# Optimization experiments

Hardware: AMD Instinct MI355X
Metric: run time of the kernel (lower is better)

Reference implementation:

```python
import jax, jax.numpy as jnp
import numpy as np

N_NODES = 50000
N_EDGES = 400000
D = 512
LN_EPS = 1e-5


def setup_inputs() -> dict:
    key = jax.random.key(0)
    k0, k1, k2, k3 = jax.random.split(key, 4)
    x = jax.random.normal(k0, (N_NODES, D), dtype=jnp.float32)
    src = jax.random.randint(k1, (N_EDGES,), 0, N_NODES, dtype=jnp.int64)
    dst = jax.random.randint(k2, (N_EDGES,), 0, N_NODES, dtype=jnp.int64)
    W = jax.random.normal(k3, (D, D), dtype=jnp.float32) * 0.05
    b = jnp.zeros((D,), dtype=jnp.float32)
    gamma = jnp.ones((D,), dtype=jnp.float32)
    beta = jnp.zeros((D,), dtype=jnp.float32)
    return {"x": x, "W": W, "b": b, "gamma": gamma, "beta": beta, "src": src, "dst": dst}


def reference(x, W, b, gamma, beta, src, dst):
    n = x.shape[0]
    ones = jnp.ones(src.shape, dtype=x.dtype)
    # DGL GraphConv norm='both': clamp degrees to >= 1
    deg_out = jnp.clip(jax.ops.segment_sum(ones, src, num_segments=n), 1.0)  # [N]
    deg_in = jnp.clip(jax.ops.segment_sum(ones, dst, num_segments=n), 1.0)   # [N]
    h = x * jax.lax.rsqrt(deg_out)[:, None]                 # [N, D] src normalization
    agg = jax.ops.segment_sum(h[src], dst, num_segments=n)  # gather->scatter-add SpMM
    h = agg * jax.lax.rsqrt(deg_in)[:, None]                # dst normalization
    h = h @ W + b                                           # dense linear
    # LayerNorm over last dim
    mu = jnp.mean(h, axis=-1, keepdims=True)
    var = jnp.mean(jnp.square(h - mu), axis=-1, keepdims=True)
    h = (h - mu) * jax.lax.rsqrt(var + LN_EPS) * gamma + beta
    # torch nn.GELU default = exact erf GELU
    return jax.nn.gelu(h, approximate=False)
```

## Files before the change

kernel.cpp:

```cpp
#include <hip/hip_runtime.h>
#include <hip/hip_bf16.h>

#define D 512

typedef __attribute__((ext_vector_type(8))) short bf16x8;
typedef __attribute__((ext_vector_type(4))) float f32x4;

__device__ inline float b2f(short h) {
    union { unsigned u; float f; } c;
    c.u = ((unsigned)(unsigned short)h) << 16;
    return c.f;
}

__device__ __forceinline__ void stage16(const void* g, void* l) {
    __builtin_amdgcn_global_load_lds((const __attribute__((address_space(1))) void*)g,
                                     (__attribute__((address_space(3))) void*)l, 16, 0, 0);
}

__global__ void k_hist(const int* __restrict__ src, const int* __restrict__ dst,
                       int* __restrict__ deg_out, int* __restrict__ deg_in, int E) {
    int e = blockIdx.x * 256 + threadIdx.x;
    if (e < E) {
        atomicAdd(&deg_out[src[e]], 1);
        atomicAdd(&deg_in[dst[e]], 1);
    }
}

__global__ __launch_bounds__(256)
void k_scale(const float* __restrict__ x, const int* __restrict__ deg_out,
             __hip_bfloat16* __restrict__ xs, int total16) {
    int i = blockIdx.x * 256 + threadIdx.x;
    if (i >= total16) return;
    int node = i >> 6;
    float w = rsqrtf((float)max(deg_out[node], 1));
    const float4* p = (const float4*)(x + (size_t)i * 8);
    float4 a = p[0], b = p[1];
    union { float4 f4; __hip_bfloat16 h[8]; } o;
    o.h[0] = __float2bfloat16(a.x * w);
    o.h[1] = __float2bfloat16(a.y * w);
    o.h[2] = __float2bfloat16(a.z * w);
    o.h[3] = __float2bfloat16(a.w * w);
    o.h[4] = __float2bfloat16(b.x * w);
    o.h[5] = __float2bfloat16(b.y * w);
    o.h[6] = __float2bfloat16(b.z * w);
    o.h[7] = __float2bfloat16(b.w * w);
    *(float4*)(xs + (size_t)i * 8) = o.f4;
}

__global__ void k_scan1(const int* __restrict__ deg_in, int* __restrict__ row_start,
                        int* __restrict__ partials, int N) {
    __shared__ int sm[1024];
    int tid = threadIdx.x;
    int i = blockIdx.x * 1024 + tid;
    int v = (i < N) ? deg_in[i] : 0;
    sm[tid] = v;
    __syncthreads();
    int acc = v;
    #pragma unroll
    for (int off = 1; off < 1024; off <<= 1) {
        int t = (tid >= off) ? sm[tid - off] : 0;
        __syncthreads();
        acc += t;
        sm[tid] = acc;
        __syncthreads();
    }
    if (i < N) row_start[i] = acc - v;
    if (tid == 1023) partials[blockIdx.x] = acc;
}

__global__ void k_scan2w(int* __restrict__ partials, int* __restrict__ row_start,
                         int nb, int N) {
    int lane = threadIdx.x;
    int orig = (lane < nb) ? partials[lane] : 0;
    int v = orig;
    #pragma unroll
    for (int off = 1; off < 64; off <<= 1) {
        int t = __shfl_up(v, off, 64);
        if (lane >= off) v += t;
    }
    if (lane < nb) partials[lane] = v - orig;
    if (lane == 63) row_start[N] = v;
}

__global__ void k_scan2s(int* __restrict__ partials, int* __restrict__ row_start,
                         int nb, int N) {
    if (threadIdx.x == 0 && blockIdx.x == 0) {
        int run = 0;
        for (int b = 0; b < nb; b++) { int t = partials[b]; partials[b] = run; run += t; }
        row_start[N] = run;
    }
}

__global__ void k_scan3(int* __restrict__ row_start, const int* __restrict__ partials, int N) {
    int i = blockIdx.x * 256 + threadIdx.x;
    if (i < N) row_start[i] += partials[i >> 10];
}

__global__ void k_fill(const int* __restrict__ src, const int* __restrict__ dst,
                       const int* __restrict__ row_start, int* __restrict__ cursor,
                       int* __restrict__ csr_src, int E) {
    int e = blockIdx.x * 256 + threadIdx.x;
    if (e < E) {
        int d = dst[e];
        int slot = atomicAdd(&cursor[d], 1);
        csr_src[row_start[d] + slot] = src[e];
    }
}

__global__ __launch_bounds__(256)
void k_spmm(const __hip_bfloat16* __restrict__ xs, const int* __restrict__ row_start,
            const int* __restrict__ csr_src, __hip_bfloat16* __restrict__ A, int N) {
    int wid = threadIdx.x >> 6;
    int lane = threadIdx.x & 63;
    int node = blockIdx.x * 4 + wid;
    if (node >= N) return;
    int rs = row_start[node], re = row_start[node + 1];

    float acc[8];
    #pragma unroll
    for (int k = 0; k < 8; k++) acc[k] = 0.f;
    const __hip_bfloat16* xl = xs + (size_t)lane * 8;

    int j = rs;
    for (; j + 4 <= re; j += 4) {
        int s0 = csr_src[j], s1 = csr_src[j + 1], s2 = csr_src[j + 2], s3 = csr_src[j + 3];
        bf16x8 v0 = *(const bf16x8*)(xl + (size_t)s0 * D);
        bf16x8 v1 = *(const bf16x8*)(xl + (size_t)s1 * D);
        bf16x8 v2 = *(const bf16x8*)(xl + (size_t)s2 * D);
        bf16x8 v3 = *(const bf16x8*)(xl + (size_t)s3 * D);
        #pragma unroll
        for (int k = 0; k < 8; k++)
            acc[k] += (b2f(v0[k]) + b2f(v1[k])) + (b2f(v2[k]) + b2f(v3[k]));
    }
    for (; j < re; j++) {
        int s = csr_src[j];
        bf16x8 v = *(const bf16x8*)(xl + (size_t)s * D);
        #pragma unroll
        for (int k = 0; k < 8; k++) acc[k] += b2f(v[k]);
    }

    float rn = rsqrtf((float)max(re - rs, 1));
    union { float4 f4; __hip_bfloat16 h[8]; } o;
    #pragma unroll
    for (int k = 0; k < 8; k++) o.h[k] = __float2bfloat16(acc[k] * rn);
    *(float4*)(A + (size_t)node * D + lane * 8) = o.f4;
}

__global__ __launch_bounds__(256)
void k_spmm_f32(const float* __restrict__ x, const int* __restrict__ row_start,
                const int* __restrict__ csr_src, const int* __restrict__ deg_out,
                __hip_bfloat16* __restrict__ A, int N) {
    int wid = threadIdx.x >> 6;
    int lane = threadIdx.x & 63;
    int node = blockIdx.x * 4 + wid;
    if (node >= N) return;
    int rs = row_start[node], re = row_start[node + 1];
    float4 acc0 = {0.f, 0.f, 0.f, 0.f};
    float4 acc1 = {0.f, 0.f, 0.f, 0.f};
    const float* xl = x + (size_t)lane * 8;
    for (int j = rs; j < re; j++) {
        int s = csr_src[j];
        float w = rsqrtf((float)max(deg_out[s], 1));
        const float4* p = (const float4*)(xl + (size_t)s * D);
        float4 a = p[0], b = p[1];
        acc0.x += a.x * w; acc0.y += a.y * w; acc0.z += a.z * w; acc0.w += a.w * w;
        acc1.x += b.x * w; acc1.y += b.y * w; acc1.z += b.z * w; acc1.w += b.w * w;
    }
    float rn = rsqrtf((float)max(re - rs, 1));
    union { float4 f4; __hip_bfloat16 h[8]; } o;
    o.h[0] = __float2bfloat16(acc0.x * rn);
    o.h[1] = __float2bfloat16(acc0.y * rn);
    o.h[2] = __float2bfloat16(acc0.z * rn);
    o.h[3] = __float2bfloat16(acc0.w * rn);
    o.h[4] = __float2bfloat16(acc1.x * rn);
    o.h[5] = __float2bfloat16(acc1.y * rn);
    o.h[6] = __float2bfloat16(acc1.z * rn);
    o.h[7] = __float2bfloat16(acc1.w * rn);
    *(float4*)(A + (size_t)node * D + lane * 8) = o.f4;
}

__global__ void k_packw(const float* __restrict__ W, __hip_bfloat16* __restrict__ Wp) {
    int tile = blockIdx.x;
    int lane = threadIdx.x;
    int kt = tile >> 5, nt = tile & 31;
    int k0 = kt * 32 + (lane >> 4) * 8;
    int n  = nt * 16 + (lane & 15);
    union { float4 f4; __hip_bfloat16 h[8]; } o;
    #pragma unroll
    for (int j = 0; j < 8; j++)
        o.h[j] = __float2bfloat16(W[(size_t)(k0 + j) * D + n]);
    *(float4*)(Wp + ((size_t)tile * 64 + lane) * 8) = o.f4;
}

__global__ __launch_bounds__(512, 4)
void k_gemm(const __hip_bfloat16* __restrict__ A, const __hip_bfloat16* __restrict__ Wp,
            const float* __restrict__ bias, const float* __restrict__ gamma,
            const float* __restrict__ beta, float* __restrict__ out, int M) {
    __shared__ __align__(16) char smem[65536];
    __shared__ float s_sum[64][4];
    __shared__ float s_sq[64][4];

    int tid = threadIdx.x;
    int wid = tid >> 6, lane = tid & 63;
    int wm = wid >> 1 & 0 ? 0 : (wid >> 2);
    wm = wid >> 2;
    int wn = wid & 3;
    int l4 = lane >> 4, coll = lane & 15;
    int bm0 = blockIdx.x * 64;

    int arow0 = bm0 + wm * 16 + coll;
    int arow1 = arow0 + 32;
    if (arow0 > M - 1) arow0 = M - 1;
    if (arow1 > M - 1) arow1 = M - 1;
    const bf16x8* a0p = (const bf16x8*)(A + (size_t)arow0 * D + l4 * 8);
    const bf16x8* a1p = (const bf16x8*)(A + (size_t)arow1 * D + l4 * 8);

    int c0 = wid * 4;
    const __hip_bfloat16* gbase = Wp + (size_t)c0 * 512 + lane * 8;
    char* lds_c0 = smem + c0 * 1024;

    f32x4 acc0[8], acc1[8];
    #pragma unroll
    for (int t = 0; t < 8; t++) { acc0[t] = (f32x4){0,0,0,0}; acc1[t] = (f32x4){0,0,0,0}; }

    #pragma unroll
    for (int r = 0; r < 4; r++)
        stage16(gbase + r * 512, lds_c0 + r * 1024);
    __syncthreads();

    for (int kt = 0; kt < 16; kt++) {
        int cur = (kt & 1) << 15;
        bf16x8 a0 = a0p[kt * 4];
        bf16x8 a1 = a1p[kt * 4];
        if (kt < 15) {
            const __hip_bfloat16* g = gbase + (size_t)(kt + 1) * 16384;
            char* lb = lds_c0 + (((kt + 1) & 1) << 15);
            #pragma unroll
            for (int r = 0; r < 4; r++)
                stage16(g + r * 512, lb + r * 1024);
        }
        #pragma unroll
        for (int t = 0; t < 8; t++) {
            bf16x8 bf = *(const bf16x8*)(smem + cur + (((wn * 8 + t) * 64 + lane) << 4));
            acc0[t] = __builtin_amdgcn_mfma_f32_16x16x32_bf16(a0, bf, acc0[t], 0, 0, 0);
            acc1[t] = __builtin_amdgcn_mfma_f32_16x16x32_bf16(a1, bf, acc1[t], 0, 0, 0);
        }
        __syncthreads();
    }

    float bia[8], gam[8], bet[8];
    #pragma unroll
    for (int t = 0; t < 8; t++) {
        int col = wn * 128 + t * 16 + coll;
        bia[t] = bias[col]; gam[t] = gamma[col]; bet[t] = beta[col];
    }
    #pragma unroll
    for (int f = 0; f < 2; f++) {
        f32x4* acc = f ? acc1 : acc0;
        #pragma unroll
        for (int r = 0; r < 4; r++) {
            float s = 0.f, q = 0.f;
            #pragma unroll
            for (int t = 0; t < 8; t++) {
                float v = acc[t][r] + bia[t];
                acc[t][r] = v;
                s += v; q += v * v;
            }
            #pragma unroll
            for (int off = 1; off < 16; off <<= 1) {
                s += __shfl_xor(s, off, 64);
                q += __shfl_xor(q, off, 64);
            }
            if (coll == 0) {
                int rb = wm * 16 + f * 32 + l4 * 4 + r;
                s_sum[rb][wn] = s;
                s_sq[rb][wn] = q;
            }
        }
    }
    __syncthreads();

    #pragma unroll
    for (int f = 0; f < 2; f++) {
        f32x4* acc = f ? acc1 : acc0;
        #pragma unroll
        for (int r = 0; r < 4; r++) {
            int rb = wm * 16 + f * 32 + l4 * 4 + r;
            int gr = bm0 + rb;
            if (gr >= M) continue;
            float s = s_sum[rb][0] + s_sum[rb][1] + s_sum[rb][2] + s_sum[rb][3];
            float q = s_sq[rb][0] + s_sq[rb][1] + s_sq[rb][2] + s_sq[rb][3];
            float mean = s * (1.0f / 512.0f);
            float var = q * (1.0f / 512.0f) - mean * mean;
            float rstd = rsqrtf(fmaxf(var, 0.f) + 1e-5f);
            float* orow = out + (size_t)gr * D + wn * 128 + coll;
            #pragma unroll
            for (int t = 0; t < 8; t++) {
                float y = (acc[t][r] - mean) * rstd * gam[t] + bet[t];
                float yy = y * y;
                float pz = fmaf(yy, -0.1029423374f, -2.3022076728f);
                float e = __builtin_amdgcn_exp2f(y * pz);
                float g = y * __builtin_amdgcn_rcpf(1.0f + e);
                orow[t * 16] = g;
            }
        }
    }
}

extern "C" void kernel_launch(void* const* d_in, const int* in_sizes, int n_in,
                              void* d_out, int out_size, void* d_ws, size_t ws_size,
                              hipStream_t stream) {
    const float* x     = (const float*)d_in[0];
    const float* W     = (const float*)d_in[1];
    const float* b     = (const float*)d_in[2];
    const float* gamma = (const float*)d_in[3];
    const float* beta  = (const float*)d_in[4];
    const int*   src   = (const int*)d_in[5];
    const int*   dst   = (const int*)d_in[6];
    int N = in_sizes[0] / D;
    int E = in_sizes[5];
    float* out = (float*)d_out;

    int* deg_out   = (int*)d_ws;
    int* deg_in    = deg_out + N;
    int* row_start = deg_in + N;
    int* cursor    = row_start + N + 1;
    int* partials  = cursor + N;
    int* csr_src   = partials + 64;
    uintptr_t p = (uintptr_t)(csr_src + E);
    p = (p + 255) & ~(uintptr_t)255;
    __hip_bfloat16* A = (__hip_bfloat16*)p;
    p += (size_t)N * D * sizeof(__hip_bfloat16);
    p = (p + 255) & ~(uintptr_t)255;
    __hip_bfloat16* Wp = (__hip_bfloat16*)p;
    p += (size_t)D * D * sizeof(__hip_bfloat16);
    p = (p + 255) & ~(uintptr_t)255;
    __hip_bfloat16* xs = (__hip_bfloat16*)p;
    size_t need_xs = (p - (uintptr_t)d_ws) + (size_t)N * D * sizeof(__hip_bfloat16);
    bool use_bf16_gather = (ws_size >= need_xs);

    hipMemsetAsync(deg_out, 0, (size_t)2 * N * sizeof(int), stream);
    hipMemsetAsync(cursor, 0, (size_t)N * sizeof(int), stream);

    k_hist<<<(E + 255) / 256, 256, 0, stream>>>(src, dst, deg_out, deg_in, E);
    int nb1 = (N + 1023) / 1024;
    k_scan1<<<nb1, 1024, 0, stream>>>(deg_in, row_start, partials, N);
    if (nb1 <= 64)
        k_scan2w<<<1, 64, 0, stream>>>(partials, row_start, nb1, N);
    else
        k_scan2s<<<1, 64, 0, stream>>>(partials, row_start, nb1, N);
    k_scan3<<<(N + 255) / 256, 256, 0, stream>>>(row_start, partials, N);
    k_fill<<<(E + 255) / 256, 256, 0, stream>>>(src, dst, row_start, cursor, csr_src, E);

    if (use_bf16_gather) {
        int total16 = N * 64;
        k_scale<<<(total16 + 255) / 256, 256, 0, stream>>>(x, deg_out, xs, total16);
        k_spmm<<<(N + 3) / 4, 256, 0, stream>>>(xs, row_start, csr_src, A, N);
    } else {
        k_spmm_f32<<<(N + 3) / 4, 256, 0, stream>>>(x, row_start, csr_src, deg_out, A, N);
    }
    k_packw<<<512, 64, 0, stream>>>(W, Wp);
    k_gemm<<<(N + 63) / 64, 512, 0, stream>>>(A, Wp, b, gamma, beta, out, N);
}
```

Baseline: 247.1 us.

## Stage A tiles through LDS and deepen GEMM prefetch pipeline with explicit waitcnts

The A operand, previously read from global memory straight into registers on every k-step, is now staged into LDS with async global_load_lds alongside W. The W/A pipeline is restructured so that two stages are in flight. LDS fragments are read into registers before a barrier, after which the next stage is issued into the freed buffer. Fine-grained s_waitcnt vmcnt plus sched_barrier replace __syncthreads, so MFMA work overlaps outstanding loads; the cost is 8KB more LDS per block and more fragile manual synchronisation.

New measurement: 238.3 us. 1.04x faster.

```diff
diff --git a/kernel.cpp b/kernel.cpp
--- a/kernel.cpp
+++ b/kernel.cpp
@@ -196,56 +196,96 @@
 void k_gemm(const __hip_bfloat16* __restrict__ A, const __hip_bfloat16* __restrict__ Wp,
             const float* __restrict__ bias, const float* __restrict__ gamma,
             const float* __restrict__ beta, float* __restrict__ out, int M) {
-    __shared__ __align__(16) char smem[65536];
+    __shared__ __align__(16) char smem[2 * 32768 + 2 * 4096];
     __shared__ float s_sum[64][4];
     __shared__ float s_sq[64][4];
+    char* smemA = smem + 65536;
 
     int tid = threadIdx.x;
     int wid = tid >> 6, lane = tid & 63;
-    int wm = wid >> 1 & 0 ? 0 : (wid >> 2);
-    wm = wid >> 2;
+    int wm = wid >> 2;
     int wn = wid & 3;
     int l4 = lane >> 4, coll = lane & 15;
     int bm0 = blockIdx.x * 64;
 
-    int arow0 = bm0 + wm * 16 + coll;
-    int arow1 = arow0 + 32;
-    if (arow0 > M - 1) arow0 = M - 1;
-    if (arow1 > M - 1) arow1 = M - 1;
-    const bf16x8* a0p = (const bf16x8*)(A + (size_t)arow0 * D + l4 * 8);
-    const bf16x8* a1p = (const bf16x8*)(A + (size_t)arow1 * D + l4 * 8);
+    int r0 = wm * 16 + coll;
+    int r1 = r0 + 32;
 
     int c0 = wid * 4;
-    const __hip_bfloat16* gbase = Wp + (size_t)c0 * 512 + lane * 8;
-    char* lds_c0 = smem + c0 * 1024;
+    const char* gw_base = (const char*)Wp + (size_t)c0 * 1024 + (size_t)lane * 16;
+    int ga_row = bm0 + lane;
+    if (ga_row > M - 1) ga_row = M - 1;
+    const char* ga_base = (const char*)A + (size_t)ga_row * 1024 + (size_t)wid * 16;
 
     f32x4 acc0[8], acc1[8];
     #pragma unroll
     for (int t = 0; t < 8; t++) { acc0[t] = (f32x4){0,0,0,0}; acc1[t] = (f32x4){0,0,0,0}; }
 
-    #pragma unroll
-    for (int r = 0; r < 4; r++)
-        stage16(gbase + r * 512, lds_c0 + r * 1024);
-    __syncthreads();
-
-    for (int kt = 0; kt < 16; kt++) {
-        int cur = (kt & 1) << 15;
-        bf16x8 a0 = a0p[kt * 4];
-        bf16x8 a1 = a1p[kt * 4];
-        if (kt < 15) {
-            const __hip_bfloat16* g = gbase + (size_t)(kt + 1) * 16384;
-            char* lb = lds_c0 + (((kt + 1) & 1) << 15);
-            #pragma unroll
-            for (int r = 0; r < 4; r++)
-                stage16(g + r * 512, lb + r * 1024);
+    auto STAGE = [&](int kt, int buf) {
+        const char* gw = gw_base + (size_t)kt * 32768;
+        char* lw = smem + buf * 32768 + c0 * 1024;
+        #pragma unroll
+        for (int r = 0; r < 4; r++)
+            stage16(gw + r * 1024, lw + r * 1024);
+        if (wid < 4)
+            stage16(ga_base + (size_t)kt * 64, smemA + buf * 4096 + wid * 1024);
+    };
+
+    STAGE(0, 0);
+    STAGE(1, 1);
+    asm volatile("s_waitcnt vmcnt(4)" ::: "memory");
+    __builtin_amdgcn_sched_barrier(0);
+    __builtin_amdgcn_s_barrier();
+
+    for (int kt = 0; kt < 14; kt++) {
+        int cur = kt & 1;
+        char* aw = smemA + cur * 4096 + l4 * 1024;
+        bf16x8 a0 = *(const bf16x8*)(aw + r0 * 16);
+        bf16x8 a1 = *(const bf16x8*)(aw + r1 * 16);
+        bf16x8 bf[8];
+        char* ww = smem + cur * 32768 + (size_t)wn * 8192 + lane * 16;
+        #pragma unroll
+        for (int t = 0; t < 8; t++)
+            bf[t] = *(const bf16x8*)(ww + t * 1024);
+        asm volatile("s_waitcnt lgkmcnt(0)" ::: "memory");
+        __builtin_amdgcn_sched_barrier(0);
+        __builtin_amdgcn_s_barrier();
+        STAGE(kt + 2, cur);
+        #pragma unroll
+        for (int t = 0; t < 8; t++) {
+            acc0[t] = __builtin_amdgcn_mfma_f32_16x16x32_bf16(a0, bf[t], acc0[t], 0, 0, 0);
+            acc1[t] = __builtin_amdgcn_mfma_f32_16x16x32_bf16(a1, bf[t], acc1[t], 0, 0, 0);
         }
+        asm volatile("s_waitcnt vmcnt(4)" ::: "memory");
+        __builtin_amdgcn_sched_barrier(0);
+        __builtin_amdgcn_s_barrier();
+    }
+    {
+        char* aw = smemA + 0 * 4096 + l4 * 1024;
+        bf16x8 a0 = *(const bf16x8*)(aw + r0 * 16);
+        bf16x8 a1 = *(const bf16x8*)(aw + r1 * 16);
+        char* ww = smem + 0 * 32768 + (size_t)wn * 8192 + lane * 16;
         #pragma unroll
         for (int t = 0; t < 8; t++) {
-            bf16x8 bf = *(const bf16x8*)(smem + cur + (((wn * 8 + t) * 64 + lane) << 4));
+            bf16x8 bf = *(const bf16x8*)(ww + t * 1024);
             acc0[t] = __builtin_amdgcn_mfma_f32_16x16x32_bf16(a0, bf, acc0[t], 0, 0, 0);
             acc1[t] = __builtin_amdgcn_mfma_f32_16x16x32_bf16(a1, bf, acc1[t], 0, 0, 0);
         }
-        __syncthreads();
+        asm volatile("s_waitcnt vmcnt(0)" ::: "memory");
+        __builtin_amdgcn_sched_barrier(0);
+        __builtin_amdgcn_s_barrier();
+    }
+    {
+        char* aw = smemA + 1 * 4096 + l4 * 1024;
+        bf16x8 a0 = *(const bf16x8*)(aw + r0 * 16);
+        bf16x8 a1 = *(const bf16x8*)(aw + r1 * 16);
+        char* ww = smem + 1 * 32768 + (size_t)wn * 8192 + lane * 16;
+        #pragma unroll
+        for (int t = 0; t < 8; t++) {
+            bf16x8 bf = *(const bf16x8*)(ww + t * 1024);
+            acc0[t] = __builtin_amdgcn_mfma_f32_16x16x32_bf16(a0, bf, acc0[t], 0, 0, 0);
+            acc1[t] = __builtin_amdgcn_mfma_f32_16x16x32_bf16(a1, bf, acc1[t], 0, 0, 0);
+        }
     }
 
     float bia[8], gam[8], bet[8];
```
